# Kernel tuning notes

Measured on AMD Instinct MI355X. Metric: run time of the kernel, lower is better.

Reference implementation:

```python
import jax, jax.numpy as jnp
import numpy as np

# static config (matches init_kwargs)
STRIDE, PAD, DIL, DG = 1, 1, 1, 1
KH, KW = 3, 3
CIN, COUT = 64, 64


def setup_inputs() -> dict:
    key = jax.random.key(0)
    k1, k2, k3, k4 = jax.random.split(key, 4)
    N, C, H, W = 4, CIN, 128, 128
    K = KH * KW
    x = jax.random.normal(k1, (N, C, H, W), dtype=jnp.float32)
    offset = jax.random.normal(k2, (N, 2 * DG * K, H, W), dtype=jnp.float32)
    mask = jax.random.uniform(k3, (N, DG * K, H, W), dtype=jnp.float32)
    stdv = 1.0 / np.sqrt(C * K)
    weight = jax.random.uniform(k4, (COUT, C, KH, KW), dtype=jnp.float32,
                                minval=-stdv, maxval=stdv)
    bias = jnp.zeros((COUT,), dtype=jnp.float32)  # no_bias=True -> frozen zeros
    return {"x": x, "offset": offset, "mask": mask, "weight": weight, "bias": bias}


def _dcnv2(x, offset, mask, weight, bias):
    N, C, H, W = x.shape
    Cout, _, kh, kw = weight.shape
    K = kh * kw
    Ho = (H + 2 * PAD - DIL * (kh - 1) - 1) // STRIDE + 1
    Wo = (W + 2 * PAD - DIL * (kw - 1) - 1) // STRIDE + 1
    Cg = C // DG

    # offsets: [N, DG, K, 2(y,x), Ho, Wo]; mask: [N, DG, K, Ho, Wo]
    off = offset.reshape(N, DG, K, 2, Ho, Wo)
    off_y, off_x = off[:, :, :, 0], off[:, :, :, 1]
    m = mask.reshape(N, DG, K, Ho, Wo)

    kidx = jnp.arange(K)
    ky, kx = kidx // kw, kidx % kw
    base_y = (jnp.arange(Ho) * STRIDE - PAD)[None, :] + (ky * DIL)[:, None]  # [K,Ho]
    base_x = (jnp.arange(Wo) * STRIDE - PAD)[None, :] + (kx * DIL)[:, None]  # [K,Wo]

    py = base_y[None, None, :, :, None].astype(x.dtype) + off_y  # [N,DG,K,Ho,Wo]
    px = base_x[None, None, :, None, :].astype(x.dtype) + off_x

    y0 = jnp.floor(py)
    x0 = jnp.floor(px)
    ly = py - y0  # frac weights
    lx = px - x0
    y0i = y0.astype(jnp.int32)
    x0i = x0.astype(jnp.int32)

    xf = x.reshape(N, DG, Cg, H * W)

    def gather(yi, xi):
        # per-corner zero padding (out-of-bounds corners contribute 0)
        valid = ((yi >= 0) & (yi < H) & (xi >= 0) & (xi < W))
        idx = jnp.clip(yi, 0, H - 1) * W + jnp.clip(xi, 0, W - 1)  # [N,DG,K,Ho,Wo]
        idx_b = jnp.broadcast_to(idx[:, :, None], (N, DG, Cg, K, Ho, Wo))
        v = jnp.take_along_axis(xf, idx_b.reshape(N, DG, Cg, -1), axis=3)
        v = v.reshape(N, DG, Cg, K, Ho, Wo)
        return v * valid[:, :, None].astype(x.dtype)

    w00 = ((1 - ly) * (1 - lx))[:, :, None]  # [N,DG,1,K,Ho,Wo]
    w01 = ((1 - ly) * lx)[:, :, None]
    w10 = (ly * (1 - lx))[:, :, None]
    w11 = (ly * lx)[:, :, None]

    val = (gather(y0i, x0i) * w00 + gather(y0i, x0i + 1) * w01
           + gather(y0i + 1, x0i) * w10 + gather(y0i + 1, x0i + 1) * w11)
    cols = val * m[:, :, None]                      # modulation
    cols = cols.reshape(N, C, K, Ho, Wo)            # DG*Cg -> C (contiguous)

    wmat = weight.reshape(Cout, C, K)
    out = jnp.einsum('nckhw,ock->nohw', cols, wmat)
    return out + bias[None, :, None, None]


def reference(x, offset, mask, weight, bias):
    return _dcnv2(x, offset, mask, weight, bias)
```

## Files before the change

### kernel.cpp

```cpp
#include <hip/hip_runtime.h>

#define N_    4
#define C_    64
#define H_    128
#define W_    128
#define KW_   3
#define K_    9
#define COUT_ 64
#define HW_   (H_ * W_)
#define NPIX  (N_ * HW_)
#define KK_   (C_ * K_)

typedef _Float16 h4 __attribute__((ext_vector_type(4)));
typedef _Float16 h8 __attribute__((ext_vector_type(8)));
typedef float v4f __attribute__((ext_vector_type(4)));
typedef int   v4i __attribute__((ext_vector_type(4)));

__global__ __launch_bounds__(256) void prep(
    const float* __restrict__ x, _Float16* __restrict__ xh,
    const float* __restrict__ w, _Float16* __restrict__ wA4)
{
    if (blockIdx.x < 1024) {
        const int n   = blockIdx.x >> 8;
        const int hw0 = (blockIdx.x & 255) * 64;

        __shared__ float tile[64][65];
        const float* xb = x + n * (C_ * HW_);
#pragma unroll
        for (int i = 0; i < 4; ++i) {
            const int idx = i * 256 + threadIdx.x;
            const int q   = idx & 15;
            const int c   = idx >> 4;
            const v4f v = *(const v4f*)&xb[c * HW_ + hw0 + 4 * q];
            tile[4 * q + 0][c] = v.x;
            tile[4 * q + 1][c] = v.y;
            tile[4 * q + 2][c] = v.z;
            tile[4 * q + 3][c] = v.w;
        }
        __syncthreads();
        _Float16* xo = xh + ((size_t)n * HW_ + hw0) * 64;
#pragma unroll
        for (int i = 0; i < 4; ++i) {
            const int idx = i * 256 + threadIdx.x;
            const int c4  = idx & 15;
            const int hr  = idx >> 4;
            h4 v;
            v.x = (_Float16)tile[hr][4 * c4 + 0];
            v.y = (_Float16)tile[hr][4 * c4 + 1];
            v.z = (_Float16)tile[hr][4 * c4 + 2];
            v.w = (_Float16)tile[hr][4 * c4 + 3];
            *(h4*)&xo[hr * 64 + 4 * c4] = v;
        }
    } else {
        const int tid = (blockIdx.x - 1024) * 256 + threadIdx.x;
        if (tid < COUT_ * KK_) {
            const int blk = tid >> 9;
            const int r   = tid & 511;
            const int l16 = r >> 5;
            const int ch  = r & 31;
            const int t   = blk >> 3;
            const int kc  = (blk >> 2) & 1;
            const int mh  = blk & 3;
            const int o   = mh * 16 + l16;
            const int c   = kc * 32 + ch;
            wA4[tid] = (_Float16)w[o * (C_ * K_) + c * K_ + t];
        }
    }
}

__global__ __launch_bounds__(256, 4) void dcn_fused(
    const _Float16* __restrict__ xh,
    const float* __restrict__ offset,
    const float* __restrict__ mask,
    const _Float16* __restrict__ wA4,
    const float* __restrict__ bias,
    float* __restrict__ out)
{
    const int tid  = threadIdx.x;
    const int lane = tid & 63;
    const int wv   = tid >> 6;
    const int quad = lane >> 4;
    const int l16  = lane & 15;
    const int g    = lane >> 3;
    const int l8   = lane & 7;

    const int lb  = (blockIdx.x & 7) * 128 + (blockIdx.x >> 3);
    const int pxb = lb * 64;
    const int n   = pxb >> 14;
    const int hwb = pxb & (HW_ - 1);

    __shared__ _Float16 cwh[576][4];
    __shared__ int      ci[576][4];
    __shared__ _Float16 Bt[2][64][72];

#pragma unroll
    for (int r = 0; r < 3; ++r) {
        const int e = tid + 256 * r;
        if (e < 576) {
            const int p  = e / 9;
            const int t  = e - p * 9;
            const int hw = hwb + p;
            const int ho = hw >> 7;
            const int wo = hw & (W_ - 1);
            const int ky = t / KW_;
            const int kx = t - ky * KW_;

            const float offy = offset[n * (2 * K_ * HW_) + (2 * t + 0) * HW_ + hw];
            const float offx = offset[n * (2 * K_ * HW_) + (2 * t + 1) * HW_ + hw];
            const float mval = mask[n * (K_ * HW_) + t * HW_ + hw];

            const float py = (float)(ho - 1 + ky) + offy;
            const float qx = (float)(wo - 1 + kx) + offx;
            const float y0f = floorf(py), x0f = floorf(qx);
            const float ly = py - y0f, lx = qx - x0f;
            const int y0 = (int)y0f, x0 = (int)x0f;
            const int y1 = y0 + 1,   x1 = x0 + 1;
            const bool vy0 = (y0 >= 0) & (y0 < H_);
            const bool vy1 = (y1 >= 0) & (y1 < H_);
            const bool vx0 = (x0 >= 0) & (x0 < W_);
            const bool vx1 = (x1 >= 0) & (x1 < W_);
            const int cy0 = min(max(y0, 0), H_ - 1);
            const int cy1 = min(max(y1, 0), H_ - 1);
            const int cx0 = min(max(x0, 0), W_ - 1);
            const int cx1 = min(max(x1, 0), W_ - 1);

            h4 q;
            q.x = (_Float16)((1.f - ly) * (1.f - lx) * mval * ((vy0 && vx0) ? 1.f : 0.f));
            q.y = (_Float16)((1.f - ly) * lx         * mval * ((vy0 && vx1) ? 1.f : 0.f));
            q.z = (_Float16)(ly         * (1.f - lx) * mval * ((vy1 && vx0) ? 1.f : 0.f));
            q.w = (_Float16)(ly         * lx         * mval * ((vy1 && vx1) ? 1.f : 0.f));
            *(h4*)&cwh[e][0] = q;
            int* qi = &ci[e][0];
            qi[0] = cy0 * W_ + cx0;
            qi[1] = cy0 * W_ + cx1;
            qi[2] = cy1 * W_ + cx0;
            qi[3] = cy1 * W_ + cx1;
        }
    }
    __syncthreads();

    const _Float16* xb8 = xh + ((size_t)n * HW_) * 64 + 8 * l8;
    const int pg  = wv * 16 + g;
    const int pg8 = pg + 8;

    const int mb   = (wv & 1) * 32;
    const int mhb  = (wv & 1) * 2;
    const int pxwl = (wv >> 1) * 32;

    const _Float16* ab = wA4 + l16 * 32 + quad * 8;

    v4f acc[2][2];
#pragma unroll
    for (int mh = 0; mh < 2; ++mh)
#pragma unroll
        for (int nh = 0; nh < 2; ++nh)
            acc[mh][nh] = (v4f){0.f, 0.f, 0.f, 0.f};

    h8 LA[2][4], LB[2][4];

#define ISSUE(t, R)                                                         \
    {                                                                       \
        const v4i oa = *(const v4i*)&ci[pg  * 9 + (t)][0];                  \
        const v4i ob = *(const v4i*)&ci[pg8 * 9 + (t)][0];                  \
        R[0][0] = *(const h8*)(xb8 + (size_t)oa.x * 64);                    \
        R[0][1] = *(const h8*)(xb8 + (size_t)oa.y * 64);                    \
        R[0][2] = *(const h8*)(xb8 + (size_t)oa.z * 64);                    \
        R[0][3] = *(const h8*)(xb8 + (size_t)oa.w * 64);                    \
        R[1][0] = *(const h8*)(xb8 + (size_t)ob.x * 64);                    \
        R[1][1] = *(const h8*)(xb8 + (size_t)ob.y * 64);                    \
        R[1][2] = *(const h8*)(xb8 + (size_t)ob.z * 64);                    \
        R[1][3] = *(const h8*)(xb8 + (size_t)ob.w * 64);                    \
    }

#define FINISH(t, R, b)                                                     \
    {                                                                       \
        _Pragma("unroll")                                                   \
        for (int h = 0; h < 2; ++h) {                                       \
            const int p = wv * 16 + h * 8 + g;                              \
            const h4 f = *(const h4*)&cwh[p * 9 + (t)][0];                  \
            const h8 F0 = {f.x, f.x, f.x, f.x, f.x, f.x, f.x, f.x};         \
            const h8 F1 = {f.y, f.y, f.y, f.y, f.y, f.y, f.y, f.y};         \
            const h8 F2 = {f.z, f.z, f.z, f.z, f.z, f.z, f.z, f.z};         \
            const h8 F3 = {f.w, f.w, f.w, f.w, f.w, f.w, f.w, f.w};         \
            h8 rr = F0 * R[h][0];                                           \
            rr = __builtin_elementwise_fma(F1, R[h][1], rr);                \
            rr = __builtin_elementwise_fma(F2, R[h][2], rr);                \
            rr = __builtin_elementwise_fma(F3, R[h][3], rr);                \
            *(h8*)&Bt[b][p][8 * l8] = rr;                                   \
        }                                                                   \
    }

#define TAP_BARRIER()                                                       \
    __builtin_amdgcn_sched_barrier(0);                                      \
    asm volatile("s_waitcnt lgkmcnt(0)");                                   \
    __builtin_amdgcn_sched_barrier(0);                                      \
    __builtin_amdgcn_s_barrier();                                           \
    __builtin_amdgcn_sched_barrier(0);

    ISSUE(0, LA)
    ISSUE(1, LB)
    FINISH(0, LA, 0)
    TAP_BARRIER()

#pragma unroll
    for (int t = 0; t < K_; ++t) {
        const int buf = t & 1;

        h8 va[2][2];
#pragma unroll
        for (int kc = 0; kc < 2; ++kc)
#pragma unroll
            for (int mh = 0; mh < 2; ++mh)
                va[kc][mh] = *(const h8*)(ab
                    + (size_t)(t * 8 + kc * 4 + (mhb + mh)) * 512);
        __builtin_amdgcn_sched_barrier(0);

        if ((t & 1) == 0) {
            if (t + 2 < K_) ISSUE(t + 2, LA)
        } else {
            if (t + 2 < K_) ISSUE(t + 2, LB)
        }
        __builtin_amdgcn_sched_barrier(0);

#pragma unroll
        for (int kc = 0; kc < 2; ++kc) {
            h8 bfr[2];
#pragma unroll
            for (int nh = 0; nh < 2; ++nh)
                bfr[nh] = *(const h8*)&Bt[buf][pxwl + nh * 16 + l16][kc * 32 + quad * 8];
#pragma unroll
            for (int mh = 0; mh < 2; ++mh)
#pragma unroll
                for (int nh = 0; nh < 2; ++nh)
                    acc[mh][nh] = __builtin_amdgcn_mfma_f32_16x16x32_f16(
                        va[kc][mh], bfr[nh], acc[mh][nh], 0, 0, 0);
        }

        if ((t & 1) == 0) {
            if (t + 1 < K_) FINISH(t + 1, LB, buf ^ 1)
        } else {
            if (t + 1 < K_) FINISH(t + 1, LA, buf ^ 1)
        }

        TAP_BARRIER()
    }
#undef ISSUE
#undef FINISH
#undef TAP_BARRIER

    float* outb = out + n * (COUT_ * HW_);
#pragma unroll
    for (int mh = 0; mh < 2; ++mh)
#pragma unroll
        for (int nh = 0; nh < 2; ++nh)
#pragma unroll
            for (int r = 0; r < 4; ++r) {
                const int m = mb + mh * 16 + quad * 4 + r;
                outb[m * HW_ + hwb + pxwl + nh * 16 + l16] = acc[mh][nh][r] + bias[m];
            }
}

__global__ __launch_bounds__(256) void dcn_fallback(
    const float* __restrict__ x, const float* __restrict__ offset,
    const float* __restrict__ mask, const float* __restrict__ wptr,
    const float* __restrict__ bias, float* __restrict__ out)
{
    const int pix = blockIdx.x * 256 + threadIdx.x;
    const int n = pix >> 14, hw = pix & (HW_ - 1);
    const int ho = hw >> 7,  wo = hw & (W_ - 1);
    float acc[COUT_];
#pragma unroll
    for (int o = 0; o < COUT_; ++o) acc[o] = bias[o];
    const float* xn   = x + n * (C_ * HW_);
    const float* offn = offset + n * (2 * K_ * HW_) + hw;
    const float* mn   = mask + n * (K_ * HW_) + hw;
    for (int ct = 0; ct < C_; ct += 8) {
        for (int k = 0; k < K_; ++k) {
            const int ky = k / KW_, kx = k - ky * KW_;
            const float off_y = offn[(2 * k + 0) * HW_];
            const float off_x = offn[(2 * k + 1) * HW_];
            const float m = mn[k * HW_];
            const float py = (float)(ho - 1 + ky) + off_y;
            const float px = (float)(wo - 1 + kx) + off_x;
            const float y0f = floorf(py), x0f = floorf(px);
            const float ly = py - y0f, lx = px - x0f;
            const int y0 = (int)y0f, x0 = (int)x0f, y1 = y0 + 1, x1 = x0 + 1;
            const bool vy0 = (y0 >= 0) & (y0 < H_), vy1 = (y1 >= 0) & (y1 < H_);
            const bool vx0 = (x0 >= 0) & (x0 < W_), vx1 = (x1 >= 0) & (x1 < W_);
            const int cy0 = min(max(y0, 0), H_ - 1), cy1 = min(max(y1, 0), H_ - 1);
            const int cx0 = min(max(x0, 0), W_ - 1), cx1 = min(max(x1, 0), W_ - 1);
            const int i00 = cy0 * W_ + cx0, i01 = cy0 * W_ + cx1;
            const int i10 = cy1 * W_ + cx0, i11 = cy1 * W_ + cx1;
            const float f00 = (1.f - ly) * (1.f - lx) * m * ((vy0 && vx0) ? 1.f : 0.f);
            const float f01 = (1.f - ly) * lx * m * ((vy0 && vx1) ? 1.f : 0.f);
            const float f10 = ly * (1.f - lx) * m * ((vy1 && vx0) ? 1.f : 0.f);
            const float f11 = ly * lx * m * ((vy1 && vx1) ? 1.f : 0.f);
            for (int cc = 0; cc < 8; ++cc) {
                const int c = ct + cc;
                const float* xc = xn + c * HW_;
                const float val = fmaf(f00, xc[i00], fmaf(f01, xc[i01],
                                  fmaf(f10, xc[i10], f11 * xc[i11])));
#pragma unroll
                for (int o = 0; o < COUT_; ++o)
                    acc[o] = fmaf(wptr[o * (C_ * K_) + c * K_ + k], val, acc[o]);
            }
        }
    }
    float* outp = out + n * (COUT_ * HW_) + hw;
#pragma unroll
    for (int o = 0; o < COUT_; ++o) outp[o * HW_] = acc[o];
}

extern "C" void kernel_launch(void* const* d_in, const int* in_sizes, int n_in,
                              void* d_out, int out_size, void* d_ws, size_t ws_size,
                              hipStream_t stream) {
    const float* x      = (const float*)d_in[0];
    const float* offset = (const float*)d_in[1];
    const float* mask   = (const float*)d_in[2];
    const float* weight = (const float*)d_in[3];
    const float* bias   = (const float*)d_in[4];
    float* out = (float*)d_out;

    const size_t xh_bytes = (size_t)NPIX * C_ * sizeof(_Float16);
    const size_t wA_bytes = (size_t)COUT_ * KK_ * sizeof(_Float16);

    if (ws_size >= xh_bytes + wA_bytes) {
        _Float16* xh  = (_Float16*)d_ws;
        _Float16* wA4 = (_Float16*)((char*)d_ws + xh_bytes);
        prep<<<1024 + 144, 256, 0, stream>>>(x, xh, weight, wA4);
        dcn_fused<<<NPIX / 64, 256, 0, stream>>>(xh, offset, mask, wA4, bias, out);
    } else {
        dcn_fallback<<<NPIX / 256, 256, 0, stream>>>(x, offset, mask, weight, bias, out);
    }
}
```

Measured before the change: 102.2 us.

## Coalesce offset/mask prologue loads and reorder tap pipeline around single barrier

The prologue now maps threads pixel-major within each tap, so consecutive lanes read consecutive offset and mask addresses instead of strided ones. The tap loop is restructured so each iteration first finishes building its own B tile, issues the next gathers, and hits one barrier before running the MFMAs. Wave priority is raised around the MFMA block. The intent is to cut uncoalesced global loads and let the gather work for the next tap overlap the matrix work. In exchange, the gather-to-use latency window changes, and the LDS writes to the coefficient tables now follow a different index pattern that may cause more bank conflicts.

```diff
diff --git a/kernel.cpp b/kernel.cpp
--- a/kernel.cpp
+++ b/kernel.cpp
@@ -93,48 +93,52 @@
     __shared__ int      ci[576][4];
     __shared__ _Float16 Bt[2][64][72];
 
-#pragma unroll
-    for (int r = 0; r < 3; ++r) {
-        const int e = tid + 256 * r;
-        if (e < 576) {
-            const int p  = e / 9;
-            const int t  = e - p * 9;
-            const int hw = hwb + p;
-            const int ho = hw >> 7;
-            const int wo = hw & (W_ - 1);
-            const int ky = t / KW_;
-            const int kx = t - ky * KW_;
-
-            const float offy = offset[n * (2 * K_ * HW_) + (2 * t + 0) * HW_ + hw];
-            const float offx = offset[n * (2 * K_ * HW_) + (2 * t + 1) * HW_ + hw];
-            const float mval = mask[n * (K_ * HW_) + t * HW_ + hw];
-
-            const float py = (float)(ho - 1 + ky) + offy;
-            const float qx = (float)(wo - 1 + kx) + offx;
-            const float y0f = floorf(py), x0f = floorf(qx);
-            const float ly = py - y0f, lx = qx - x0f;
-            const int y0 = (int)y0f, x0 = (int)x0f;
-            const int y1 = y0 + 1,   x1 = x0 + 1;
-            const bool vy0 = (y0 >= 0) & (y0 < H_);
-            const bool vy1 = (y1 >= 0) & (y1 < H_);
-            const bool vx0 = (x0 >= 0) & (x0 < W_);
-            const bool vx1 = (x1 >= 0) & (x1 < W_);
-            const int cy0 = min(max(y0, 0), H_ - 1);
-            const int cy1 = min(max(y1, 0), H_ - 1);
-            const int cx0 = min(max(x0, 0), W_ - 1);
-            const int cx1 = min(max(x1, 0), W_ - 1);
-
-            h4 q;
-            q.x = (_Float16)((1.f - ly) * (1.f - lx) * mval * ((vy0 && vx0) ? 1.f : 0.f));
-            q.y = (_Float16)((1.f - ly) * lx         * mval * ((vy0 && vx1) ? 1.f : 0.f));
-            q.z = (_Float16)(ly         * (1.f - lx) * mval * ((vy1 && vx0) ? 1.f : 0.f));
-            q.w = (_Float16)(ly         * lx         * mval * ((vy1 && vx1) ? 1.f : 0.f));
-            *(h4*)&cwh[e][0] = q;
-            int* qi = &ci[e][0];
-            qi[0] = cy0 * W_ + cx0;
-            qi[1] = cy0 * W_ + cx1;
-            qi[2] = cy1 * W_ + cx0;
-            qi[3] = cy1 * W_ + cx1;
+    {
+        const int p  = tid & 63;
+        const int q  = tid >> 6;
+        const int hw = hwb + p;
+        const int ho = hw >> 7;
+        const int wo = hw & (W_ - 1);
+        const float* offp = offset + n * (2 * K_ * HW_) + hw;
+        const float* mp   = mask   + n * (K_ * HW_) + hw;
+#pragma unroll
+        for (int j = 0; j < 3; ++j) {
+            const int t = q + 4 * j;
+            if (t < K_) {
+                const int ky = t / KW_;
+                const int kx = t - ky * KW_;
+                const float offy = offp[(2 * t + 0) * HW_];
+                const float offx = offp[(2 * t + 1) * HW_];
+                const float mval = mp[t * HW_];
+
+                const float py = (float)(ho - 1 + ky) + offy;
+                const float qx = (float)(wo - 1 + kx) + offx;
+                const float y0f = floorf(py), x0f = floorf(qx);
+                const float ly = py - y0f, lx = qx - x0f;
+                const int y0 = (int)y0f, x0 = (int)x0f;
+                const int y1 = y0 + 1,   x1 = x0 + 1;
+                const bool vy0 = (y0 >= 0) & (y0 < H_);
+                const bool vy1 = (y1 >= 0) & (y1 < H_);
+                const bool vx0 = (x0 >= 0) & (x0 < W_);
+                const bool vx1 = (x1 >= 0) & (x1 < W_);
+                const int cy0 = min(max(y0, 0), H_ - 1);
+                const int cy1 = min(max(y1, 0), H_ - 1);
+                const int cx0 = min(max(x0, 0), W_ - 1);
+                const int cx1 = min(max(x1, 0), W_ - 1);
+
+                const int e = p * 9 + t;
+                h4 qq;
+                qq.x = (_Float16)((1.f - ly) * (1.f - lx) * mval * ((vy0 && vx0) ? 1.f : 0.f));
+                qq.y = (_Float16)((1.f - ly) * lx         * mval * ((vy0 && vx1) ? 1.f : 0.f));
+                qq.z = (_Float16)(ly         * (1.f - lx) * mval * ((vy1 && vx0) ? 1.f : 0.f));
+                qq.w = (_Float16)(ly         * lx         * mval * ((vy1 && vx1) ? 1.f : 0.f));
+                *(h4*)&cwh[e][0] = qq;
+                int* qi = &ci[e][0];
+                qi[0] = cy0 * W_ + cx0;
+                qi[1] = cy0 * W_ + cx1;
+                qi[2] = cy1 * W_ + cx0;
+                qi[3] = cy1 * W_ + cx1;
+            }
         }
     }
     __syncthreads();
@@ -199,12 +203,18 @@
 
     ISSUE(0, LA)
     ISSUE(1, LB)
-    FINISH(0, LA, 0)
-    TAP_BARRIER()
+    __builtin_amdgcn_sched_barrier(0);
 
 #pragma unroll
     for (int t = 0; t < K_; ++t) {
         const int buf = t & 1;
+
+        if ((t & 1) == 0) {
+            FINISH(t, LA, buf)
+        } else {
+            FINISH(t, LB, buf)
+        }
+        __builtin_amdgcn_sched_barrier(0);
 
         h8 va[2][2];
 #pragma unroll
@@ -220,8 +230,10 @@
         } else {
             if (t + 2 < K_) ISSUE(t + 2, LB)
         }
-        __builtin_amdgcn_sched_barrier(0);
-
+
+        TAP_BARRIER()
+
+        __builtin_amdgcn_s_setprio(1);
 #pragma unroll
         for (int kc = 0; kc < 2; ++kc) {
             h8 bfr[2];
@@ -235,14 +247,8 @@
                     acc[mh][nh] = __builtin_amdgcn_mfma_f32_16x16x32_f16(
                         va[kc][mh], bfr[nh], acc[mh][nh], 0, 0, 0);
         }
-
-        if ((t & 1) == 0) {
-            if (t + 1 < K_) FINISH(t + 1, LB, buf ^ 1)
-        } else {
-            if (t + 1 < K_) FINISH(t + 1, LA, buf ^ 1)
-        }
-
-        TAP_BARRIER()
+        __builtin_amdgcn_s_setprio(0);
+        __builtin_amdgcn_sched_barrier(0);
     }
 #undef ISSUE
 #undef FINISH
```

New measurement: 100.6 us. Within noise of the previous version (-1.6%).
